# Optimization experiments

Hardware: AMD Instinct MI355X
Metric: run time of the kernel (lower is better)

The kernel has to match this reference:

```python
import jax, jax.numpy as jnp
import numpy as np

VOCAB = 32000
DIM = 1024
CTX = 4          # local_context_size
EPS = 1e-6       # linear-attention denominator eps
LN_EPS = 1e-5    # LayerNorm eps


def setup_inputs() -> dict:
    key = jax.random.key(0)
    ks = jax.random.split(key, 12)
    s = 0.02
    inp = {
        "x": jax.random.randint(ks[0], (2, 2048), 0, VOCAB),
        "embedding": jax.random.normal(ks[1], (VOCAB, DIM), jnp.float32) * s,
        "Wq": jax.random.normal(ks[2], (DIM, DIM), jnp.float32) * s,
        "bq": jnp.zeros((DIM,), jnp.float32),
        "Wk": jax.random.normal(ks[3], (DIM, DIM), jnp.float32) * s,
        "bk": jnp.zeros((DIM,), jnp.float32),
        "Wv": jax.random.normal(ks[4], (DIM, DIM), jnp.float32) * s,
        "bv": jnp.zeros((DIM,), jnp.float32),
        "Wo": jax.random.normal(ks[5], (DIM, DIM), jnp.float32) * s,
        "bo": jnp.zeros((DIM,), jnp.float32),
        "ln_gamma": jnp.ones((DIM,), jnp.float32),
        "ln_beta": jnp.zeros((DIM,), jnp.float32),
        "Wout": jax.random.normal(ks[6], (DIM, VOCAB), jnp.float32) * s,
        "bout": jnp.zeros((VOCAB,), jnp.float32),
    }
    return inp


def _feature_map(x):
    # F.elu(x) + 1.0
    return jax.nn.elu(x) + 1.0


def _local_context_sum(emb):
    # sum of emb shifted right by 0..CTX-1 (zeros padded at front)
    out = emb
    for off in range(1, CTX):
        out = out + jnp.pad(emb, ((0, 0), (off, 0), (0, 0)))[:, :-off, :]
    return out


def reference(x, embedding, Wq, bq, Wk, bk, Wv, bv, Wo, bo,
              ln_gamma, ln_beta, Wout, bout):
    emb = embedding[x]                       # [B,S,D]
    emb = _local_context_sum(emb)

    q = _feature_map(emb @ Wq + bq)          # [B,S,D], strictly positive
    k = _feature_map(emb @ Wk + bk)
    v = emb @ Wv + bv

    S = emb.shape[1]
    # Causal linear attention. Equivalent to the per-step recurrence:
    #   num_t = q_t . (sum_{s<=t} k_s v_s^T);  den_t = q_t . (sum_{s<=t} k_s)
    scores = jnp.einsum("bsd,btd->bst", q, k)            # [B,S,S]
    mask = jnp.tril(jnp.ones((S, S), scores.dtype))
    scores = scores * mask
    num = jnp.einsum("bst,bte->bse", scores, v)          # [B,S,D]
    den = jnp.sum(scores, axis=-1, keepdims=True) + EPS  # [B,S,1]
    attn = num / den

    out = attn @ Wo + bo                     # dsra out_proj

    # LayerNorm
    mu = jnp.mean(out, axis=-1, keepdims=True)
    var = jnp.mean(jnp.square(out - mu), axis=-1, keepdims=True)
    out = (out - mu) * jax.lax.rsqrt(var + LN_EPS) * ln_gamma + ln_beta

    logits = out @ Wout + bout               # [B,S,VOCAB]
    return logits
```

## Files before the change

### kernel.cpp

```cpp
#include <hip/hip_runtime.h>
#include <cstddef>

#define DIM   1024
#define VOCAB 32000
#define BATCH 2
#define SEQ   2048
#define CTX   4
#define EPS_D 1e-6f
#define LN_EPS 1e-5f

typedef __bf16 bf16x8 __attribute__((ext_vector_type(8)));
typedef float  f32x4  __attribute__((ext_vector_type(4)));
typedef unsigned short ushortx8 __attribute__((ext_vector_type(8)));

__device__ __forceinline__ unsigned short f2bf(float f) {
    unsigned u = __float_as_uint(f);
    u += 0x7fffu + ((u >> 16) & 1u);
    return (unsigned short)(u >> 16);
}
__device__ __forceinline__ float bf2f(unsigned short h) {
    return __uint_as_float((unsigned)h << 16);
}

#define GL16(gp, lp) __builtin_amdgcn_global_load_lds(                        \
    (const __attribute__((address_space(1))) void*)(gp),                      \
    (__attribute__((address_space(3))) void*)(lp), 16, 0, 0)

__global__ __launch_bounds__(256)
void embed_split_kernel(const int* __restrict__ x,
                        const float* __restrict__ table,
                        ushort* __restrict__ eh,
                        ushort* __restrict__ el) {
    int bs = blockIdx.x;
    int b = bs >> 11;
    int s = bs & (SEQ - 1);
    int d = threadIdx.x * 4;
    float4 acc = make_float4(0.f, 0.f, 0.f, 0.f);
    #pragma unroll
    for (int o = 0; o < CTX; ++o) {
        int ss = s - o;
        if (ss >= 0) {
            int row = x[b * SEQ + ss];
            const float4 v = *(const float4*)&table[(size_t)row * DIM + d];
            acc.x += v.x; acc.y += v.y; acc.z += v.z; acc.w += v.w;
        }
    }
    ushort4 h, l;
    h.x = f2bf(acc.x); l.x = f2bf(acc.x - bf2f(h.x));
    h.y = f2bf(acc.y); l.y = f2bf(acc.y - bf2f(h.y));
    h.z = f2bf(acc.z); l.z = f2bf(acc.z - bf2f(h.z));
    h.w = f2bf(acc.w); l.w = f2bf(acc.w - bf2f(h.w));
    *(ushort4*)&eh[(size_t)bs * DIM + d] = h;
    *(ushort4*)&el[(size_t)bs * DIM + d] = l;
}

__global__ __launch_bounds__(256)
void embed_ctx_kernel(const int* __restrict__ x,
                      const float* __restrict__ table,
                      float* __restrict__ emb) {
    int bs = blockIdx.x;
    int b = bs >> 11;
    int s = bs & (SEQ - 1);
    int d = threadIdx.x * 4;
    float4 acc = make_float4(0.f, 0.f, 0.f, 0.f);
    #pragma unroll
    for (int o = 0; o < CTX; ++o) {
        int ss = s - o;
        if (ss >= 0) {
            int row = x[b * SEQ + ss];
            const float4 v = *(const float4*)&table[(size_t)row * DIM + d];
            acc.x += v.x; acc.y += v.y; acc.z += v.z; acc.w += v.w;
        }
    }
    *(float4*)&emb[(size_t)bs * DIM + d] = acc;
}

__global__ __launch_bounds__(256)
void tsplit_kernel(const float* __restrict__ W,
                   ushort* __restrict__ th,
                   ushort* __restrict__ tl,
                   int K, int N) {
    __shared__ float tile[32][129];
    const int n0 = blockIdx.x * 32;
    const int k0 = blockIdx.y * 128;
    const int t = threadIdx.x;

    #pragma unroll
    for (int it = 0; it < 4; ++it) {
        int kk = it * 32 + (t >> 3);
        int nn = (t & 7) * 4;
        float4 v4 = *(const float4*)&W[(size_t)(k0 + kk) * N + n0 + nn];
        tile[nn + 0][kk] = v4.x;
        tile[nn + 1][kk] = v4.y;
        tile[nn + 2][kk] = v4.z;
        tile[nn + 3][kk] = v4.w;
    }
    __syncthreads();

    #pragma unroll
    for (int it = 0; it < 2; ++it) {
        int u = it * 256 + t;
        int nn = u >> 4;
        int kc = (u & 15) * 8;
        ushortx8 h, l;
        #pragma unroll
        for (int j = 0; j < 8; ++j) {
            float f = tile[nn][kc + j];
            unsigned short hb = f2bf(f);
            h[j] = hb;
            l[j] = f2bf(f - bf2f(hb));
        }
        size_t off = (size_t)(n0 + nn) * K + k0 + kc;
        *(ushortx8*)&th[off] = h;
        *(ushortx8*)&tl[off] = l;
    }
}

template<int ACT, bool HASB, bool HASDIV, bool CAUSAL, bool TRIK, int OM>
__global__ __launch_bounds__(256, 2)
void mfma3_kernel(const ushort* __restrict__ Ah, const ushort* __restrict__ Al,
                  const ushort* __restrict__ Bh, const ushort* __restrict__ Bl,
                  const float* __restrict__ bias, const float* __restrict__ denp,
                  float* __restrict__ Cf, ushort* __restrict__ Ch, ushort* __restrict__ Cl,
                  int M, int N, int K,
                  long long aBat, long long bBat, long long cBat, long long dBat) {
    __shared__ __align__(16) ushort sAh[4096];
    __shared__ __align__(16) ushort sAl[4096];
    __shared__ __align__(16) ushort sBh[4096];
    __shared__ __align__(16) ushort sBl[4096];

    const int tid = threadIdx.x;
    const int zb = blockIdx.y;
    Ah += (size_t)zb * aBat;  Al += (size_t)zb * aBat;
    Bh += (size_t)zb * bBat;  Bl += (size_t)zb * bBat;
    if (OM == 0) { Cf += (size_t)zb * cBat; }
    else         { Ch += (size_t)zb * cBat; Cl += (size_t)zb * cBat; }
    if (HASDIV) denp += (size_t)zb * dBat;

    const int ntn = N >> 7;
    const int mbase = (blockIdx.x / ntn) << 7;
    const int nbase = (blockIdx.x % ntn) << 7;

    if (CAUSAL && nbase > mbase + 127) {
        ushortx8 z = {0, 0, 0, 0, 0, 0, 0, 0};
        for (int u = tid * 8; u < 128 * 128; u += 2048) {
            int rr = u >> 7, cc = u & 127;
            size_t off = (size_t)(mbase + rr) * N + nbase + cc;
            *(ushortx8*)&Ch[off] = z;
            *(ushortx8*)&Cl[off] = z;
        }
        return;
    }

    const int srl = tid >> 2;
    const int schunk = (tid & 3) ^ ((tid >> 3) & 3);
    const size_t skofs = (size_t)schunk * 8;

    const ushort* gAh0 = Ah + (size_t)(mbase + srl) * K + skofs;
    const ushort* gAh1 = Ah + (size_t)(mbase + 64 + srl) * K + skofs;
    const ushort* gAl0 = Al + (size_t)(mbase + srl) * K + skofs;
    const ushort* gAl1 = Al + (size_t)(mbase + 64 + srl) * K + skofs;
    const ushort* gBh0 = Bh + (size_t)(nbase + srl) * K + skofs;
    const ushort* gBh1 = Bh + (size_t)(nbase + 64 + srl) * K + skofs;
    const ushort* gBl0 = Bl + (size_t)(nbase + srl) * K + skofs;
    const ushort* gBl1 = Bl + (size_t)(nbase + 64 + srl) * K + skofs;

    const int l0 = tid * 8;
    const int l1 = 2048 + tid * 8;

    const int lane = tid & 63;
    const int wid = tid >> 6;
    const int wr = (wid >> 1) * 64;
    const int wc = (wid & 1) * 64;
    const int lrow = lane & 15;
    const int g = lane >> 4;
    int aoff[4], boff[4];
    #pragma unroll
    for (int i = 0; i < 4; ++i) {
        int r = wr + i * 16 + lrow;
        aoff[i] = r * 32 + ((g ^ ((r >> 1) & 3)) << 3);
        int rn = wc + i * 16 + lrow;
        boff[i] = rn * 32 + ((g ^ ((rn >> 1) & 3)) << 3);
    }

    f32x4 acc[4][4];
    #pragma unroll
    for (int i = 0; i < 4; ++i)
        #pragma unroll
        for (int j = 0; j < 4; ++j)
            acc[i][j] = (f32x4){0.f, 0.f, 0.f, 0.f};

    const int ktiles = TRIK ? ((mbase + 128) >> 5) : (K >> 5);
    for (int kt = 0; kt < ktiles; ++kt) {
        GL16(gAh0, sAh + l0);  GL16(gAh1, sAh + l1);
        GL16(gAl0, sAl + l0);  GL16(gAl1, sAl + l1);
        GL16(gBh0, sBh + l0);  GL16(gBh1, sBh + l1);
        GL16(gBl0, sBl + l0);  GL16(gBl1, sBl + l1);
        gAh0 += 32; gAh1 += 32; gAl0 += 32; gAl1 += 32;
        gBh0 += 32; gBh1 += 32; gBl0 += 32; gBl1 += 32;
        __syncthreads();

        bf16x8 fBh[4], fBl[4];
        #pragma unroll
        for (int i = 0; i < 4; ++i) {
            fBh[i] = *(const bf16x8*)(sBh + boff[i]);
            fBl[i] = *(const bf16x8*)(sBl + boff[i]);
        }
        #pragma unroll
        for (int mi = 0; mi < 4; ++mi) {
            bf16x8 ah = *(const bf16x8*)(sAh + aoff[mi]);
            bf16x8 al = *(const bf16x8*)(sAl + aoff[mi]);
            #pragma unroll
            for (int ni = 0; ni < 4; ++ni) {
                acc[mi][ni] = __builtin_amdgcn_mfma_f32_16x16x32_bf16(ah, fBh[ni], acc[mi][ni], 0, 0, 0);
                acc[mi][ni] = __builtin_amdgcn_mfma_f32_16x16x32_bf16(ah, fBl[ni], acc[mi][ni], 0, 0, 0);
                acc[mi][ni] = __builtin_amdgcn_mfma_f32_16x16x32_bf16(al, fBh[ni], acc[mi][ni], 0, 0, 0);
            }
        }
        __syncthreads();
    }

    #pragma unroll
    for (int ni = 0; ni < 4; ++ni) {
        const int c = nbase + wc + ni * 16 + lrow;
        float bv = 0.f;
        if (HASB) bv = bias[c];
        #pragma unroll
        for (int mi = 0; mi < 4; ++mi) {
            if (OM == 2) {
                const int r0 = mbase + wr + mi * 16 + g * 4;
                ushort4 h4, l4;
                #pragma unroll
                for (int rg = 0; rg < 4; ++rg) {
                    float vv = acc[mi][ni][rg];
                    if (HASB) vv += bv;
                    if (ACT == 1) vv = (vv > 0.f) ? (vv + 1.f) : __expf(vv);
                    unsigned short hb = f2bf(vv);
                    ((unsigned short*)&h4)[rg] = hb;
                    ((unsigned short*)&l4)[rg] = f2bf(vv - bf2f(hb));
                }
                *(ushort4*)&Ch[(size_t)c * M + r0] = h4;
                *(ushort4*)&Cl[(size_t)c * M + r0] = l4;
            } else {
                #pragma unroll
                for (int rg = 0; rg < 4; ++rg) {
                    const int r = mbase + wr + mi * 16 + g * 4 + rg;
                    float vv = acc[mi][ni][rg];
                    if (HASDIV) vv /= denp[r];
                    if (HASB) vv += bv;
                    if (ACT == 1) vv = (vv > 0.f) ? (vv + 1.f) : __expf(vv);
                    if (CAUSAL && c > r) vv = 0.f;
                    if (OM == 0) {
                        Cf[(size_t)r * N + c] = vv;
                    } else {
                        unsigned short hb = f2bf(vv);
                        Ch[(size_t)r * N + c] = hb;
                        Cl[(size_t)r * N + c] = f2bf(vv - bf2f(hb));
                    }
                }
            }
        }
    }
}

__device__ __forceinline__ float block_reduce_sum(float v, float* red) {
    #pragma unroll
    for (int off = 32; off > 0; off >>= 1) v += __shfl_down(v, off);
    const int lane = threadIdx.x & 63;
    const int wid = threadIdx.x >> 6;
    if (lane == 0) red[wid] = v;
    __syncthreads();
    float s = red[0] + red[1] + red[2] + red[3];
    return s;
}

__global__ __launch_bounds__(256)
void den_bf_kernel(const ushort* __restrict__ sh,
                   const ushort* __restrict__ sl,
                   float* __restrict__ den) {
    const int row = blockIdx.x;
    const int b = row >> 11;
    const int i = row & (SEQ - 1);
    const size_t base = (size_t)b * SEQ * SEQ + (size_t)i * SEQ;
    const int j = threadIdx.x * 8;
    ushortx8 h = *(const ushortx8*)&sh[base + j];
    ushortx8 l = *(const ushortx8*)&sl[base + j];
    float s = 0.f;
    #pragma unroll
    for (int t = 0; t < 8; ++t) s += bf2f(h[t]) + bf2f(l[t]);
    __shared__ float red[4];
    float tot = block_reduce_sum(s, red);
    if (threadIdx.x == 0) den[row] = tot + EPS_D;
}

__global__ __launch_bounds__(256)
void den_kernel(const float* __restrict__ scores, float* __restrict__ den) {
    const int row = blockIdx.x;
    const int b = row >> 11;
    const int i = row & (SEQ - 1);
    const float* r = scores + (size_t)b * SEQ * SEQ + (size_t)i * SEQ;
    float s = 0.f;
    for (int j = threadIdx.x * 4; j < SEQ; j += 256 * 4) {
        float4 v = *(const float4*)&r[j];
        s += v.x + v.y + v.z + v.w;
    }
    __shared__ float red[4];
    float tot = block_reduce_sum(s, red);
    if (threadIdx.x == 0) den[row] = tot + EPS_D;
}

__global__ __launch_bounds__(256)
void ln_split_kernel(const float* __restrict__ io,
                     const float* __restrict__ gamma,
                     const float* __restrict__ beta,
                     ushort* __restrict__ ahi,
                     ushort* __restrict__ alo) {
    const size_t row = blockIdx.x;
    const float* r = io + row * DIM;
    const int d = threadIdx.x * 4;
    float4 v = *(const float4*)&r[d];
    float s = v.x + v.y + v.z + v.w;
    float sq = v.x * v.x + v.y * v.y + v.z * v.z + v.w * v.w;
    __shared__ float r1[4];
    __shared__ float r2[4];
    float tot = block_reduce_sum(s, r1);
    __syncthreads();
    float totsq = block_reduce_sum(sq, r2);
    const float mu = tot * (1.f / DIM);
    const float var = totsq * (1.f / DIM) - mu * mu;
    const float rs = rsqrtf(var + LN_EPS);
    float4 gv = *(const float4*)&gamma[d];
    float4 bv = *(const float4*)&beta[d];
    v.x = (v.x - mu) * rs * gv.x + bv.x;
    v.y = (v.y - mu) * rs * gv.y + bv.y;
    v.z = (v.z - mu) * rs * gv.z + bv.z;
    v.w = (v.w - mu) * rs * gv.w + bv.w;
    ushort4 h, l;
    h.x = f2bf(v.x); l.x = f2bf(v.x - bf2f(h.x));
    h.y = f2bf(v.y); l.y = f2bf(v.y - bf2f(h.y));
    h.z = f2bf(v.z); l.z = f2bf(v.z - bf2f(h.z));
    h.w = f2bf(v.w); l.w = f2bf(v.w - bf2f(h.w));
    *(ushort4*)&ahi[row * DIM + d] = h;
    *(ushort4*)&alo[row * DIM + d] = l;
}

__global__ __launch_bounds__(256)
void ln_kernel(float* __restrict__ io,
               const float* __restrict__ gamma,
               const float* __restrict__ beta) {
    const size_t row = blockIdx.x;
    float* r = io + row * DIM;
    const int d = threadIdx.x * 4;
    float4 v = *(const float4*)&r[d];
    float s = v.x + v.y + v.z + v.w;
    float sq = v.x * v.x + v.y * v.y + v.z * v.z + v.w * v.w;
    __shared__ float r1[4];
    __shared__ float r2[4];
    float tot = block_reduce_sum(s, r1);
    __syncthreads();
    float totsq = block_reduce_sum(sq, r2);
    const float mu = tot * (1.f / DIM);
    const float var = totsq * (1.f / DIM) - mu * mu;
    const float rs = rsqrtf(var + LN_EPS);
    float4 gv = *(const float4*)&gamma[d];
    float4 bv = *(const float4*)&beta[d];
    v.x = (v.x - mu) * rs * gv.x + bv.x;
    v.y = (v.y - mu) * rs * gv.y + bv.y;
    v.z = (v.z - mu) * rs * gv.z + bv.z;
    v.w = (v.w - mu) * rs * gv.w + bv.w;
    *(float4*)&r[d] = v;
}

__global__ __launch_bounds__(256, 2)
void logits_mfma_kernel(const ushort* __restrict__ Ahi,
                        const ushort* __restrict__ Alo,
                        const ushort* __restrict__ Bhi,
                        const ushort* __restrict__ Blo,
                        const float* __restrict__ bias,
                        float* __restrict__ C) {
    __shared__ __align__(16) ushort sAh[4096];
    __shared__ __align__(16) ushort sAl[4096];
    __shared__ __align__(16) ushort sBh[4096];
    __shared__ __align__(16) ushort sBl[4096];

    const int tid = threadIdx.x;
    const int bid = blockIdx.x;
    const int swz = (bid & 7) * 1000 + (bid >> 3);
    const int mbase = (swz & 31) * 128;
    const int nbase = (swz >> 5) * 128;

    const int srl = tid >> 2;
    const int schunk = (tid & 3) ^ ((tid >> 3) & 3);
    const size_t skofs = (size_t)schunk * 8;

    const ushort* gAh0 = Ahi + (size_t)(mbase + srl) * DIM + skofs;
    const ushort* gAh1 = Ahi + (size_t)(mbase + 64 + srl) * DIM + skofs;
    const ushort* gAl0 = Alo + (size_t)(mbase + srl) * DIM + skofs;
    const ushort* gAl1 = Alo + (size_t)(mbase + 64 + srl) * DIM + skofs;
    const ushort* gBh0 = Bhi + (size_t)(nbase + srl) * DIM + skofs;
    const ushort* gBh1 = Bhi + (size_t)(nbase + 64 + srl) * DIM + skofs;
    const ushort* gBl0 = Blo + (size_t)(nbase + srl) * DIM + skofs;
    const ushort* gBl1 = Blo + (size_t)(nbase + 64 + srl) * DIM + skofs;

    const int l0 = tid * 8;
    const int l1 = 2048 + tid * 8;

    const int lane = tid & 63;
    const int wid = tid >> 6;
    const int wr = (wid >> 1) * 64;
    const int wc = (wid & 1) * 64;
    const int lrow = lane & 15;
    const int g = lane >> 4;
    int aoff[4], boff[4];
    #pragma unroll
    for (int i = 0; i < 4; ++i) {
        int r = wr + i * 16 + lrow;
        aoff[i] = r * 32 + ((g ^ ((r >> 1) & 3)) << 3);
        int rn = wc + i * 16 + lrow;
        boff[i] = rn * 32 + ((g ^ ((rn >> 1) & 3)) << 3);
    }

    f32x4 acc[4][4];
    #pragma unroll
    for (int i = 0; i < 4; ++i)
        #pragma unroll
        for (int j = 0; j < 4; ++j)
            acc[i][j] = (f32x4){0.f, 0.f, 0.f, 0.f};

    for (int kt = 0; kt < DIM / 32; ++kt) {
        GL16(gAh0, sAh + l0);  GL16(gAh1, sAh + l1);
        GL16(gAl0, sAl + l0);  GL16(gAl1, sAl + l1);
        GL16(gBh0, sBh + l0);  GL16(gBh1, sBh + l1);
        GL16(gBl0, sBl + l0);  GL16(gBl1, sBl + l1);
        gAh0 += 32; gAh1 += 32; gAl0 += 32; gAl1 += 32;
        gBh0 += 32; gBh1 += 32; gBl0 += 32; gBl1 += 32;
        __syncthreads();

        bf16x8 fBh[4], fBl[4];
        #pragma unroll
        for (int i = 0; i < 4; ++i) {
            fBh[i] = *(const bf16x8*)(sBh + boff[i]);
            fBl[i] = *(const bf16x8*)(sBl + boff[i]);
        }
        #pragma unroll
        for (int mi = 0; mi < 4; ++mi) {
            bf16x8 ah = *(const bf16x8*)(sAh + aoff[mi]);
            bf16x8 al = *(const bf16x8*)(sAl + aoff[mi]);
            #pragma unroll
            for (int ni = 0; ni < 4; ++ni) {
                acc[mi][ni] = __builtin_amdgcn_mfma_f32_16x16x32_bf16(ah, fBh[ni], acc[mi][ni], 0, 0, 0);
                acc[mi][ni] = __builtin_amdgcn_mfma_f32_16x16x32_bf16(ah, fBl[ni], acc[mi][ni], 0, 0, 0);
                acc[mi][ni] = __builtin_amdgcn_mfma_f32_16x16x32_bf16(al, fBh[ni], acc[mi][ni], 0, 0, 0);
            }
        }
        __syncthreads();
    }

    #pragma unroll
    for (int ni = 0; ni < 4; ++ni) {
        const int c = nbase + wc + ni * 16 + lrow;
        const float bv = bias[c];
        #pragma unroll
        for (int mi = 0; mi < 4; ++mi) {
            #pragma unroll
            for (int rg = 0; rg < 4; ++rg) {
                const int r = mbase + wr + mi * 16 + g * 4 + rg;
                __builtin_nontemporal_store(acc[mi][ni][rg] + bv,
                                            &C[(size_t)r * VOCAB + c]);
            }
        }
    }
}

template<int ACT, bool HAS_BIAS, bool HAS_DIV>
__global__ __launch_bounds__(256)
void gemm_kernel(const float* __restrict__ A,
                 const float* __restrict__ B,
                 const float* __restrict__ bias,
                 const float* __restrict__ rowdiv,
                 float* __restrict__ C,
                 int M, int N, int K) {
    __shared__ float As[16][64];
    __shared__ float Bs[16][64];

    const int tid = threadIdx.x;
    const int tx = tid & 15;
    const int ty = tid >> 4;
    const int row0 = blockIdx.y * 64;
    const int col0 = blockIdx.x * 64;

    const int a_row = tid >> 2;
    const int a_col = (tid & 3) * 4;
    const int b_row = tid >> 4;
    const int b_col = (tid & 15) * 4;

    const float* Aptr = A + (size_t)(row0 + a_row) * K + a_col;
    const float* Bptr = B + (size_t)b_row * N + col0 + b_col;

    float acc[4][4];
    #pragma unroll
    for (int i = 0; i < 4; ++i)
        #pragma unroll
        for (int j = 0; j < 4; ++j) acc[i][j] = 0.f;

    for (int k0 = 0; k0 < K; k0 += 16) {
        float4 a4 = *(const float4*)(Aptr + k0);
        float4 b4 = *(const float4*)(Bptr + (size_t)k0 * N);
        As[a_col + 0][a_row] = a4.x;
        As[a_col + 1][a_row] = a4.y;
        As[a_col + 2][a_row] = a4.z;
        As[a_col + 3][a_row] = a4.w;
        *(float4*)&Bs[b_row][b_col] = b4;
        __syncthreads();
        #pragma unroll
        for (int kk = 0; kk < 16; ++kk) {
            float4 av = *(const float4*)&As[kk][ty * 4];
            float4 bv = *(const float4*)&Bs[kk][tx * 4];
            float am[4] = {av.x, av.y, av.z, av.w};
            float bm[4] = {bv.x, bv.y, bv.z, bv.w};
            #pragma unroll
            for (int i = 0; i < 4; ++i)
                #pragma unroll
                for (int j = 0; j < 4; ++j)
                    acc[i][j] = fmaf(am[i], bm[j], acc[i][j]);
        }
        __syncthreads();
    }

    #pragma unroll
    for (int i = 0; i < 4; ++i) {
        const int r = row0 + ty * 4 + i;
        float rdiv = 1.f;
        if (HAS_DIV) rdiv = 1.f / rowdiv[r];
        #pragma unroll
        for (int j = 0; j < 4; ++j) {
            const int c = col0 + tx * 4 + j;
            float v = acc[i][j] * rdiv;
            if (HAS_BIAS) v += bias[c];
            if (ACT == 1) v = (v > 0.f) ? (v + 1.f) : __expf(v);
            C[(size_t)r * N + c] = v;
        }
    }
}

__global__ __launch_bounds__(256)
void scores_kernel(const float* __restrict__ q,
                   const float* __restrict__ k,
                   float* __restrict__ scores) {
    const int b = blockIdx.z;
    const int tid = threadIdx.x;
    const int tx = tid & 15;
    const int ty = tid >> 4;
    const int i0 = blockIdx.y * 64;
    const int j0 = blockIdx.x * 64;
    float* Sc = scores + (size_t)b * SEQ * SEQ;

    if (j0 > i0 + 63) {
        #pragma unroll
        for (int i = 0; i < 4; ++i)
            #pragma unroll
            for (int j = 0; j < 4; ++j)
                Sc[(size_t)(i0 + ty * 4 + i) * SEQ + j0 + tx * 4 + j] = 0.f;
        return;
    }

    const float* Q = q + (size_t)b * SEQ * DIM;
    const float* Kp = k + (size_t)b * SEQ * DIM;

    __shared__ float Qs[16][64];
    __shared__ float Ks[16][64];

    const int l_row = tid >> 2;
    const int l_col = (tid & 3) * 4;

    const float* Qptr = Q + (size_t)(i0 + l_row) * DIM + l_col;
    const float* Kptr = Kp + (size_t)(j0 + l_row) * DIM + l_col;

    float acc[4][4];
    #pragma unroll
    for (int i = 0; i < 4; ++i)
        #pragma unroll
        for (int j = 0; j < 4; ++j) acc[i][j] = 0.f;

    for (int d0 = 0; d0 < DIM; d0 += 16) {
        float4 a4 = *(const float4*)(Qptr + d0);
        float4 b4 = *(const float4*)(Kptr + d0);
        Qs[l_col + 0][l_row] = a4.x;
        Qs[l_col + 1][l_row] = a4.y;
        Qs[l_col + 2][l_row] = a4.z;
        Qs[l_col + 3][l_row] = a4.w;
        Ks[l_col + 0][l_row] = b4.x;
        Ks[l_col + 1][l_row] = b4.y;
        Ks[l_col + 2][l_row] = b4.z;
        Ks[l_col + 3][l_row] = b4.w;
        __syncthreads();
        #pragma unroll
        for (int kk = 0; kk < 16; ++kk) {
            float4 av = *(const float4*)&Qs[kk][ty * 4];
            float4 bv = *(const float4*)&Ks[kk][tx * 4];
            float am[4] = {av.x, av.y, av.z, av.w};
            float bm[4] = {bv.x, bv.y, bv.z, bv.w};
            #pragma unroll
            for (int i = 0; i < 4; ++i)
                #pragma unroll
                for (int j = 0; j < 4; ++j)
                    acc[i][j] = fmaf(am[i], bm[j], acc[i][j]);
        }
        __syncthreads();
    }

    #pragma unroll
    for (int i = 0; i < 4; ++i) {
        const int ii = i0 + ty * 4 + i;
        #pragma unroll
        for (int j = 0; j < 4; ++j) {
            const int jj = j0 + tx * 4 + j;
            Sc[(size_t)ii * SEQ + jj] = (jj <= ii) ? acc[i][j] : 0.f;
        }
    }
}

extern "C" void kernel_launch(void* const* d_in, const int* in_sizes, int n_in,
                              void* d_out, int out_size, void* d_ws, size_t ws_size,
                              hipStream_t stream) {
    const int*   x     = (const int*)d_in[0];
    const float* table = (const float*)d_in[1];
    const float* Wq    = (const float*)d_in[2];
    const float* bq    = (const float*)d_in[3];
    const float* Wk    = (const float*)d_in[4];
    const float* bk    = (const float*)d_in[5];
    const float* Wv    = (const float*)d_in[6];
    const float* bv    = (const float*)d_in[7];
    const float* Wo    = (const float*)d_in[8];
    const float* bo    = (const float*)d_in[9];
    const float* gamma = (const float*)d_in[10];
    const float* beta  = (const float*)d_in[11];
    const float* Wout  = (const float*)d_in[12];
    const float* bout  = (const float*)d_in[13];
    float* logits = (float*)d_out;

    const int M = BATCH * SEQ;

    char* p = (char*)d_ws;
    auto alloc = [&](size_t bytes) { char* r = p; p += bytes; return r; };
    ushort* WoutTh = (ushort*)alloc((size_t)VOCAB * DIM * 2);
    ushort* WoutTl = (ushort*)alloc((size_t)VOCAB * DIM * 2);
    ushort* ehi    = (ushort*)alloc((size_t)M * DIM * 2);
    ushort* elo    = (ushort*)alloc((size_t)M * DIM * 2);
    ushort* WqTh   = (ushort*)alloc((size_t)DIM * DIM * 2);
    ushort* WqTl   = (ushort*)alloc((size_t)DIM * DIM * 2);
    ushort* WkTh   = (ushort*)alloc((size_t)DIM * DIM * 2);
    ushort* WkTl   = (ushort*)alloc((size_t)DIM * DIM * 2);
    ushort* WvTh   = (ushort*)alloc((size_t)DIM * DIM * 2);
    ushort* WvTl   = (ushort*)alloc((size_t)DIM * DIM * 2);
    ushort* WoTh   = (ushort*)alloc((size_t)DIM * DIM * 2);
    ushort* WoTl   = (ushort*)alloc((size_t)DIM * DIM * 2);
    ushort* qhi    = (ushort*)alloc((size_t)M * DIM * 2);
    ushort* qlo    = (ushort*)alloc((size_t)M * DIM * 2);
    ushort* khi    = (ushort*)alloc((size_t)M * DIM * 2);
    ushort* klo    = (ushort*)alloc((size_t)M * DIM * 2);
    ushort* vTh    = (ushort*)alloc((size_t)BATCH * DIM * SEQ * 2);
    ushort* vTl    = (ushort*)alloc((size_t)BATCH * DIM * SEQ * 2);
    ushort* shi    = (ushort*)alloc((size_t)BATCH * SEQ * SEQ * 2);
    ushort* slo    = (ushort*)alloc((size_t)BATCH * SEQ * SEQ * 2);
    float*  den    = (float*)alloc((size_t)M * 4);
    const size_t need = (size_t)(p - (char*)d_ws);

    ushort* attnh = qhi;
    ushort* attnl = qlo;
    float*  outf  = (float*)khi;
    ushort* ahi   = ehi;
    ushort* alo   = elo;

    if (ws_size >= need) {
        tsplit_kernel<<<dim3(DIM / 32, DIM / 128), 256, 0, stream>>>(Wq, WqTh, WqTl, DIM, DIM);
        tsplit_kernel<<<dim3(DIM / 32, DIM / 128), 256, 0, stream>>>(Wk, WkTh, WkTl, DIM, DIM);
        tsplit_kernel<<<dim3(DIM / 32, DIM / 128), 256, 0, stream>>>(Wv, WvTh, WvTl, DIM, DIM);
        tsplit_kernel<<<dim3(DIM / 32, DIM / 128), 256, 0, stream>>>(Wo, WoTh, WoTl, DIM, DIM);
        tsplit_kernel<<<dim3(VOCAB / 32, DIM / 128), 256, 0, stream>>>(Wout, WoutTh, WoutTl, DIM, VOCAB);

        embed_split_kernel<<<M, 256, 0, stream>>>(x, table, ehi, elo);

        mfma3_kernel<1, true, false, false, false, 1>
            <<<dim3((M / 128) * (DIM / 128), 1), 256, 0, stream>>>(
            ehi, elo, WqTh, WqTl, bq, nullptr, nullptr, qhi, qlo,
            M, DIM, DIM, 0, 0, 0, 0);
        mfma3_kernel<1, true, false, false, false, 1>
            <<<dim3((M / 128) * (DIM / 128), 1), 256, 0, stream>>>(
            ehi, elo, WkTh, WkTl, bk, nullptr, nullptr, khi, klo,
            M, DIM, DIM, 0, 0, 0, 0);
        mfma3_kernel<0, true, false, false, false, 2>
            <<<dim3((SEQ / 128) * (DIM / 128), BATCH), 256, 0, stream>>>(
            ehi, elo, WvTh, WvTl, bv, nullptr, nullptr, vTh, vTl,
            SEQ, DIM, DIM,
            (long long)SEQ * DIM, 0, (long long)DIM * SEQ, 0);

        mfma3_kernel<0, false, false, true, false, 1>
            <<<dim3((SEQ / 128) * (SEQ / 128), BATCH), 256, 0, stream>>>(
            qhi, qlo, khi, klo, nullptr, nullptr, nullptr, shi, slo,
            SEQ, SEQ, DIM,
            (long long)SEQ * DIM, (long long)SEQ * DIM, (long long)SEQ * SEQ, 0);
        den_bf_kernel<<<M, 256, 0, stream>>>(shi, slo, den);

        mfma3_kernel<0, false, true, false, true, 1>
            <<<dim3((SEQ / 128) * (DIM / 128), BATCH), 256, 0, stream>>>(
            shi, slo, vTh, vTl, nullptr, den, nullptr, attnh, attnl,
            SEQ, DIM, SEQ,
            (long long)SEQ * SEQ, (long long)DIM * SEQ, (long long)SEQ * DIM,
            (long long)SEQ);

        mfma3_kernel<0, true, false, false, false, 0>
            <<<dim3((M / 128) * (DIM / 128), 1), 256, 0, stream>>>(
            attnh, attnl, WoTh, WoTl, bo, nullptr, outf, nullptr, nullptr,
            M, DIM, DIM, 0, 0, 0, 0);

        ln_split_kernel<<<M, 256, 0, stream>>>(outf, gamma, beta, ahi, alo);

        logits_mfma_kernel<<<(M / 128) * (VOCAB / 128), 256, 0, stream>>>(
            ahi, alo, WoutTh, WoutTl, bout, logits);
    } else {
        const size_t NE = (size_t)M * DIM;
        float* ws    = (float*)d_ws;
        float* emb   = ws;
        float* q     = ws + NE;
        float* k     = ws + 2 * NE;
        float* v     = ws + 3 * NE;
        float* sc    = ws + 4 * NE;
        float* denf  = sc + (size_t)BATCH * SEQ * SEQ;
        float* attn  = emb;
        float* out   = q;

        embed_ctx_kernel<<<M, 256, 0, stream>>>(x, table, emb);
        dim3 gq(DIM / 64, M / 64);
        gemm_kernel<1, true, false><<<gq, 256, 0, stream>>>(emb, Wq, bq, nullptr, q, M, DIM, DIM);
        gemm_kernel<1, true, false><<<gq, 256, 0, stream>>>(emb, Wk, bk, nullptr, k, M, DIM, DIM);
        gemm_kernel<0, true, false><<<gq, 256, 0, stream>>>(emb, Wv, bv, nullptr, v, M, DIM, DIM);
        dim3 gs(SEQ / 64, SEQ / 64, BATCH);
        scores_kernel<<<gs, 256, 0, stream>>>(q, k, sc);
        den_kernel<<<M, 256, 0, stream>>>(sc, denf);
        dim3 gn(DIM / 64, SEQ / 64);
        for (int b = 0; b < BATCH; ++b) {
            gemm_kernel<0, false, true><<<gn, 256, 0, stream>>>(
                sc + (size_t)b * SEQ * SEQ, v + (size_t)b * SEQ * DIM,
                nullptr, denf + (size_t)b * SEQ,
                attn + (size_t)b * SEQ * DIM, SEQ, DIM, SEQ);
        }
        gemm_kernel<0, true, false><<<gq, 256, 0, stream>>>(attn, Wo, bo, nullptr, out, M, DIM, DIM);
        ln_kernel<<<M, 256, 0, stream>>>(out, gamma, beta);
        dim3 gl(VOCAB / 64, M / 64);
        gemm_kernel<0, true, false><<<gl, 256, 0, stream>>>(out, Wout, bout, nullptr, logits, M, VOCAB, DIM);
    }
}
```

Baseline: 1.855 ms.

## Fuse QKV projections and weight splits; skip causal zero tiles; retile logits swizzle

Merges the Q, K and V projection GEMMs into one kernel over a concatenated weight and fuses the four small weight split launches into one grid. The causal score GEMM no longer writes zeros for fully masked tiles, and the denominator reduction sums only the elements at or below the diagonal instead of relying on stored zeros. The logits GEMM block-to-tile mapping is changed to group M tiles per XCD. The aim is fewer launches, less write traffic and better L2 locality, at the cost of extra code and reliance on downstream kernels never reading the unwritten score tiles.

```diff
diff --git a/kernel.cpp b/kernel.cpp
--- a/kernel.cpp
+++ b/kernel.cpp
@@ -75,11 +75,10 @@
     *(float4*)&emb[(size_t)bs * DIM + d] = acc;
 }
 
-__global__ __launch_bounds__(256)
-void tsplit_kernel(const float* __restrict__ W,
-                   ushort* __restrict__ th,
-                   ushort* __restrict__ tl,
-                   int K, int N) {
+__device__ __forceinline__ void tsplit_body(const float* __restrict__ W,
+                                            ushort* __restrict__ th,
+                                            ushort* __restrict__ tl,
+                                            int K, int N) {
     __shared__ float tile[32][129];
     const int n0 = blockIdx.x * 32;
     const int k0 = blockIdx.y * 128;
@@ -114,6 +113,26 @@
         *(ushortx8*)&th[off] = h;
         *(ushortx8*)&tl[off] = l;
     }
+}
+
+__global__ __launch_bounds__(256)
+void tsplit_kernel(const float* __restrict__ W,
+                   ushort* __restrict__ th,
+                   ushort* __restrict__ tl,
+                   int K, int N) {
+    tsplit_body(W, th, tl, K, N);
+}
+
+__global__ __launch_bounds__(256)
+void tsplit4_kernel(const float* __restrict__ Wq, const float* __restrict__ Wk,
+                    const float* __restrict__ Wv, const float* __restrict__ Wo,
+                    ushort* __restrict__ qkvTh, ushort* __restrict__ qkvTl,
+                    ushort* __restrict__ WoTh,  ushort* __restrict__ WoTl) {
+    const int z = blockIdx.z;
+    const float* W = (z == 0) ? Wq : (z == 1) ? Wk : (z == 2) ? Wv : Wo;
+    ushort* th = (z < 3) ? qkvTh + (size_t)z * DIM * DIM : WoTh;
+    ushort* tl = (z < 3) ? qkvTl + (size_t)z * DIM * DIM : WoTl;
+    tsplit_body(W, th, tl, DIM, DIM);
 }
 
 template<int ACT, bool HASB, bool HASDIV, bool CAUSAL, bool TRIK, int OM>
@@ -141,16 +160,7 @@
     const int mbase = (blockIdx.x / ntn) << 7;
     const int nbase = (blockIdx.x % ntn) << 7;
 
-    if (CAUSAL && nbase > mbase + 127) {
-        ushortx8 z = {0, 0, 0, 0, 0, 0, 0, 0};
-        for (int u = tid * 8; u < 128 * 128; u += 2048) {
-            int rr = u >> 7, cc = u & 127;
-            size_t off = (size_t)(mbase + rr) * N + nbase + cc;
-            *(ushortx8*)&Ch[off] = z;
-            *(ushortx8*)&Cl[off] = z;
-        }
-        return;
-    }
+    if (CAUSAL && nbase > mbase + 127) return;
 
     const int srl = tid >> 2;
     const int schunk = (tid & 3) ^ ((tid >> 3) & 3);
@@ -227,37 +237,148 @@
         if (HASB) bv = bias[c];
         #pragma unroll
         for (int mi = 0; mi < 4; ++mi) {
-            if (OM == 2) {
+            #pragma unroll
+            for (int rg = 0; rg < 4; ++rg) {
+                const int r = mbase + wr + mi * 16 + g * 4 + rg;
+                float vv = acc[mi][ni][rg];
+                if (HASDIV) vv /= denp[r];
+                if (HASB) vv += bv;
+                if (ACT == 1) vv = (vv > 0.f) ? (vv + 1.f) : __expf(vv);
+                if (CAUSAL && c > r) vv = 0.f;
+                if (OM == 0) {
+                    Cf[(size_t)r * N + c] = vv;
+                } else {
+                    unsigned short hb = f2bf(vv);
+                    Ch[(size_t)r * N + c] = hb;
+                    Cl[(size_t)r * N + c] = f2bf(vv - bf2f(hb));
+                }
+            }
+        }
+    }
+}
+
+__global__ __launch_bounds__(256, 2)
+void qkvproj_kernel(const ushort* __restrict__ Ah, const ushort* __restrict__ Al,
+                    const ushort* __restrict__ Bh, const ushort* __restrict__ Bl,
+                    const float* __restrict__ bq, const float* __restrict__ bk,
+                    const float* __restrict__ bv_,
+                    ushort* __restrict__ qh, ushort* __restrict__ ql,
+                    ushort* __restrict__ kh, ushort* __restrict__ kl,
+                    ushort* __restrict__ vTh, ushort* __restrict__ vTl) {
+    __shared__ __align__(16) ushort sAh[4096];
+    __shared__ __align__(16) ushort sAl[4096];
+    __shared__ __align__(16) ushort sBh[4096];
+    __shared__ __align__(16) ushort sBl[4096];
+
+    const int tid = threadIdx.x;
+    const int ntn = 24;
+    const int mbase = (blockIdx.x / ntn) << 7;
+    const int nbase = (blockIdx.x % ntn) << 7;
+    const int mode = nbase >> 10;
+    const int cb = nbase & 1023;
+
+    const int srl = tid >> 2;
+    const int schunk = (tid & 3) ^ ((tid >> 3) & 3);
+    const size_t skofs = (size_t)schunk * 8;
+
+    const ushort* gAh0 = Ah + (size_t)(mbase + srl) * DIM + skofs;
+    const ushort* gAh1 = Ah + (size_t)(mbase + 64 + srl) * DIM + skofs;
+    const ushort* gAl0 = Al + (size_t)(mbase + srl) * DIM + skofs;
+    const ushort* gAl1 = Al + (size_t)(mbase + 64 + srl) * DIM + skofs;
+    const ushort* gBh0 = Bh + (size_t)(nbase + srl) * DIM + skofs;
+    const ushort* gBh1 = Bh + (size_t)(nbase + 64 + srl) * DIM + skofs;
+    const ushort* gBl0 = Bl + (size_t)(nbase + srl) * DIM + skofs;
+    const ushort* gBl1 = Bl + (size_t)(nbase + 64 + srl) * DIM + skofs;
+
+    const int l0 = tid * 8;
+    const int l1 = 2048 + tid * 8;
+
+    const int lane = tid & 63;
+    const int wid = tid >> 6;
+    const int wr = (wid >> 1) * 64;
+    const int wc = (wid & 1) * 64;
+    const int lrow = lane & 15;
+    const int g = lane >> 4;
+    int aoff[4], boff[4];
+    #pragma unroll
+    for (int i = 0; i < 4; ++i) {
+        int r = wr + i * 16 + lrow;
+        aoff[i] = r * 32 + ((g ^ ((r >> 1) & 3)) << 3);
+        int rn = wc + i * 16 + lrow;
+        boff[i] = rn * 32 + ((g ^ ((rn >> 1) & 3)) << 3);
+    }
+
+    f32x4 acc[4][4];
+    #pragma unroll
+    for (int i = 0; i < 4; ++i)
+        #pragma unroll
+        for (int j = 0; j < 4; ++j)
+            acc[i][j] = (f32x4){0.f, 0.f, 0.f, 0.f};
+
+    for (int kt = 0; kt < DIM / 32; ++kt) {
+        GL16(gAh0, sAh + l0);  GL16(gAh1, sAh + l1);
+        GL16(gAl0, sAl + l0);  GL16(gAl1, sAl + l1);
+        GL16(gBh0, sBh + l0);  GL16(gBh1, sBh + l1);
+        GL16(gBl0, sBl + l0);  GL16(gBl1, sBl + l1);
+        gAh0 += 32; gAh1 += 32; gAl0 += 32; gAl1 += 32;
+        gBh0 += 32; gBh1 += 32; gBl0 += 32; gBl1 += 32;
+        __syncthreads();
+
+        bf16x8 fBh[4], fBl[4];
+        #pragma unroll
+        for (int i = 0; i < 4; ++i) {
+            fBh[i] = *(const bf16x8*)(sBh + boff[i]);
+            fBl[i] = *(const bf16x8*)(sBl + boff[i]);
+        }
+        #pragma unroll
+        for (int mi = 0; mi < 4; ++mi) {
+            bf16x8 ah = *(const bf16x8*)(sAh + aoff[mi]);
+            bf16x8 al = *(const bf16x8*)(sAl + aoff[mi]);
+            #pragma unroll
+            for (int ni = 0; ni < 4; ++ni) {
+                acc[mi][ni] = __builtin_amdgcn_mfma_f32_16x16x32_bf16(ah, fBh[ni], acc[mi][ni], 0, 0, 0);
+                acc[mi][ni] = __builtin_amdgcn_mfma_f32_16x16x32_bf16(ah, fBl[ni], acc[mi][ni], 0, 0, 0);
+                acc[mi][ni] = __builtin_amdgcn_mfma_f32_16x16x32_bf16(al, fBh[ni], acc[mi][ni], 0, 0, 0);
+            }
+        }
+        __syncthreads();
+    }
+
+    const float* bias = (mode == 0) ? bq : (mode == 1) ? bk : bv_;
+    ushort* dh = (mode == 0) ? qh : kh;
+    ushort* dl = (mode == 0) ? ql : kl;
+
+    #pragma unroll
+    for (int ni = 0; ni < 4; ++ni) {
+        const int c = cb + wc + ni * 16 + lrow;
+        const float bvv = bias[c];
+        #pragma unroll
+        for (int mi = 0; mi < 4; ++mi) {
+            if (mode < 2) {
+                #pragma unroll
+                for (int rg = 0; rg < 4; ++rg) {
+                    const int r = mbase + wr + mi * 16 + g * 4 + rg;
+                    float vv = acc[mi][ni][rg] + bvv;
+                    vv = (vv > 0.f) ? (vv + 1.f) : __expf(vv);
+                    unsigned short hb = f2bf(vv);
+                    dh[(size_t)r * DIM + c] = hb;
+                    dl[(size_t)r * DIM + c] = f2bf(vv - bf2f(hb));
+                }
+            } else {
                 const int r0 = mbase + wr + mi * 16 + g * 4;
+                const int batch = r0 >> 11;
+                const int s0 = r0 & (SEQ - 1);
                 ushort4 h4, l4;
                 #pragma unroll
                 for (int rg = 0; rg < 4; ++rg) {
-                    float vv = acc[mi][ni][rg];
-                    if (HASB) vv += bv;
-                    if (ACT == 1) vv = (vv > 0.f) ? (vv + 1.f) : __expf(vv);
+                    float vv = acc[mi][ni][rg] + bvv;
                     unsigned short hb = f2bf(vv);
                     ((unsigned short*)&h4)[rg] = hb;
                     ((unsigned short*)&l4)[rg] = f2bf(vv - bf2f(hb));
                 }
-                *(ushort4*)&Ch[(size_t)c * M + r0] = h4;
-                *(ushort4*)&Cl[(size_t)c * M + r0] = l4;
-            } else {
-                #pragma unroll
-                for (int rg = 0; rg < 4; ++rg) {
-                    const int r = mbase + wr + mi * 16 + g * 4 + rg;
-                    float vv = acc[mi][ni][rg];
-                    if (HASDIV) vv /= denp[r];
-                    if (HASB) vv += bv;
-                    if (ACT == 1) vv = (vv > 0.f) ? (vv + 1.f) : __expf(vv);
-                    if (CAUSAL && c > r) vv = 0.f;
-                    if (OM == 0) {
-                        Cf[(size_t)r * N + c] = vv;
-                    } else {
-                        unsigned short hb = f2bf(vv);
-                        Ch[(size_t)r * N + c] = hb;
-                        Cl[(size_t)r * N + c] = f2bf(vv - bf2f(hb));
-                    }
-                }
+                size_t off = (size_t)batch * DIM * SEQ + (size_t)c * SEQ + s0;
+                *(ushort4*)&vTh[off] = h4;
+                *(ushort4*)&vTl[off] = l4;
             }
         }
     }
@@ -286,8 +407,9 @@
     ushortx8 h = *(const ushortx8*)&sh[base + j];
     ushortx8 l = *(const ushortx8*)&sl[base + j];
     float s = 0.f;
-    #pragma unroll
-    for (int t = 0; t < 8; ++t) s += bf2f(h[t]) + bf2f(l[t]);
+    int lim = i - j;
+    if (lim > 7) lim = 7;
+    for (int t = 0; t <= lim; ++t) s += bf2f(h[t]) + bf2f(l[t]);
     __shared__ float red[4];
     float tot = block_reduce_sum(s, red);
     if (threadIdx.x == 0) den[row] = tot + EPS_D;
@@ -385,9 +507,10 @@
 
     const int tid = threadIdx.x;
     const int bid = blockIdx.x;
-    const int swz = (bid & 7) * 1000 + (bid >> 3);
-    const int mbase = (swz & 31) * 128;
-    const int nbase = (swz >> 5) * 128;
+    const int xcd = bid & 7;
+    const int idx = bid >> 3;
+    const int mbase = ((xcd << 2) | (idx & 3)) * 128;
+    const int nbase = (idx >> 2) * 128;
 
     const int srl = tid >> 2;
     const int schunk = (tid & 3) ^ ((tid >> 3) & 3);
@@ -647,12 +770,8 @@
     ushort* WoutTl = (ushort*)alloc((size_t)VOCAB * DIM * 2);
     ushort* ehi    = (ushort*)alloc((size_t)M * DIM * 2);
     ushort* elo    = (ushort*)alloc((size_t)M * DIM * 2);
-    ushort* WqTh   = (ushort*)alloc((size_t)DIM * DIM * 2);
-    ushort* WqTl   = (ushort*)alloc((size_t)DIM * DIM * 2);
-    ushort* WkTh   = (ushort*)alloc((size_t)DIM * DIM * 2);
-    ushort* WkTl   = (ushort*)alloc((size_t)DIM * DIM * 2);
-    ushort* WvTh   = (ushort*)alloc((size_t)DIM * DIM * 2);
-    ushort* WvTl   = (ushort*)alloc((size_t)DIM * DIM * 2);
+    ushort* WqkvTh = (ushort*)alloc((size_t)3 * DIM * DIM * 2);
+    ushort* WqkvTl = (ushort*)alloc((size_t)3 * DIM * DIM * 2);
     ushort* WoTh   = (ushort*)alloc((size_t)DIM * DIM * 2);
     ushort* WoTl   = (ushort*)alloc((size_t)DIM * DIM * 2);
     ushort* qhi    = (ushort*)alloc((size_t)M * DIM * 2);
@@ -673,27 +792,16 @@
     ushort* alo   = elo;
 
     if (ws_size >= need) {
-        tsplit_kernel<<<dim3(DIM / 32, DIM / 128), 256, 0, stream>>>(Wq, WqTh, WqTl, DIM, DIM);
-        tsplit_kernel<<<dim3(DIM / 32, DIM / 128), 256, 0, stream>>>(Wk, WkTh, WkTl, DIM, DIM);
-        tsplit_kernel<<<dim3(DIM / 32, DIM / 128), 256, 0, stream>>>(Wv, WvTh, WvTl, DIM, DIM);
-        tsplit_kernel<<<dim3(DIM / 32, DIM / 128), 256, 0, stream>>>(Wo, WoTh, WoTl, DIM, DIM);
-        tsplit_kernel<<<dim3(VOCAB / 32, DIM / 128), 256, 0, stream>>>(Wout, WoutTh, WoutTl, DIM, VOCAB);
+        tsplit4_kernel<<<dim3(DIM / 32, DIM / 128, 4), 256, 0, stream>>>(
+            Wq, Wk, Wv, Wo, WqkvTh, WqkvTl, WoTh, WoTl);
+        tsplit_kernel<<<dim3(VOCAB / 32, DIM / 128), 256, 0, stream>>>(
+            Wout, WoutTh, WoutTl, DIM, VOCAB);
 
         embed_split_kernel<<<M, 256, 0, stream>>>(x, table, ehi, elo);
 
-        mfma3_kernel<1, true, false, false, false, 1>
-            <<<dim3((M / 128) * (DIM / 128), 1), 256, 0, stream>>>(
-            ehi, elo, WqTh, WqTl, bq, nullptr, nullptr, qhi, qlo,
-            M, DIM, DIM, 0, 0, 0, 0);
-        mfma3_kernel<1, true, false, false, false, 1>
-            <<<dim3((M / 128) * (DIM / 128), 1), 256, 0, stream>>>(
-            ehi, elo, WkTh, WkTl, bk, nullptr, nullptr, khi, klo,
-            M, DIM, DIM, 0, 0, 0, 0);
-        mfma3_kernel<0, true, false, false, false, 2>
-            <<<dim3((SEQ / 128) * (DIM / 128), BATCH), 256, 0, stream>>>(
-            ehi, elo, WvTh, WvTl, bv, nullptr, nullptr, vTh, vTl,
-            SEQ, DIM, DIM,
-            (long long)SEQ * DIM, 0, (long long)DIM * SEQ, 0);
+        qkvproj_kernel<<<(M / 128) * 24, 256, 0, stream>>>(
+            ehi, elo, WqkvTh, WqkvTl, bq, bk, bv,
+            qhi, qlo, khi, klo, vTh, vTl);
 
         mfma3_kernel<0, false, false, true, false, 1>
             <<<dim3((SEQ / 128) * (SEQ / 128), BATCH), 256, 0, stream>>>(
```

Result: faster. 1.584 ms (-14.6%).
